# Performance work log

Hardware: AMD Instinct MI355X
Metric: run time of the kernel (lower is better)

Reference implementation:

```python
import jax, jax.numpy as jnp
import numpy as np

B, L = 16, 54            # dialogues, utterances per dialogue
NDIM = 512; H = 512; NS = 2
T = B * L                # 864 utterances
N = 3 * T                # 2592 nodes (l,a,v per utterance)
NE = B * (L + 3)         # 912 hyperedges (3 modality + L utterance per dialogue)
NNZ = 6 * T              # 5184 incidence entries
E = B * 3 * L * (L - 1)  # 137376 directed intra-modality edges
NUM_L = 3; NUM_K = 4
EPS = 1e-8


def _build_indices():
    rng = np.random.default_rng(0)
    spk = rng.integers(0, NS, size=(B, L))
    # qmask [L, B, NS] one-hot of speakers (matches torch argmax path)
    qmask = np.eye(NS, dtype=np.float32)[spk].transpose(1, 0, 2)
    ar = np.arange(L)
    i1, i2, ht = [], [], []
    for d in range(B):
        base = d * 3 * L
        nl = base + ar; na = nl + L; nv = nl + 2 * L
        # 3 modality hyperedges then L per-utterance (l,a,v) hyperedges
        i1 += [nl, na, nv, np.stack([nl, na, nv], 1).reshape(-1)]
        eb = d * (L + 3)
        i2 += [np.repeat(eb + np.arange(3), L), np.repeat(eb + 3 + ar, 3)]
        ht += [np.ones(L, np.int64), np.zeros(3, np.int64)]
    hyperedge_index = np.stack([np.concatenate(i1), np.concatenate(i2)]).astype(np.int64)
    hyperedge_type = np.concatenate(ht)
    # full permutation edges within each modality of each dialogue
    s0 = np.repeat(ar, L); d0 = np.tile(ar, L)
    m = s0 != d0; s0, d0 = s0[m], d0[m]
    src, dst, et = [], [], []
    for d in range(B):
        same = (spk[d][s0] == spk[d][d0]).astype(np.int64)
        for mm in range(3):
            off = d * 3 * L + mm * L
            src.append(s0 + off); dst.append(d0 + off); et.append(same)
    edge_index = np.stack([np.concatenate(src), np.concatenate(dst)]).astype(np.int64)
    edge_type = np.concatenate(et)
    return qmask, hyperedge_index, hyperedge_type, edge_index, edge_type


def setup_inputs() -> dict:
    key = jax.random.key(0)
    ks = jax.random.split(key, 16)
    qmask, hei, het, ei, et = _build_indices()
    n = lambda k, s: jax.random.normal(k, s, dtype=jnp.float32)
    inp = {
        'a': n(ks[0], (T, NDIM)), 'v': n(ks[1], (T, NDIM)), 'l': n(ks[2], (T, NDIM)),
        'qmask': jnp.asarray(qmask),
        'spk_emb': n(ks[3], (NS, NDIM)) * 0.05,
        'fc1_W': n(ks[4], (NDIM, H)) * 0.05, 'fc1_b': jnp.zeros((H,), jnp.float32),
        'he_weight': jnp.ones((NE,), jnp.float32),
        'ew_weight': jnp.ones((NNZ,), jnp.float32),
        'he_attr1': jax.random.uniform(ks[5], (H,), dtype=jnp.float32),
        'he_attr2': jax.random.uniform(ks[6], (H,), dtype=jnp.float32),
        'hc_W': n(ks[7], (NUM_L, H, H)) * 0.05, 'hc_b': jnp.zeros((NUM_L, H), jnp.float32),
        'm3_W0': n(ks[8], (NUM_K, H, H)) * 0.05,
        'm3_W1': n(ks[9], (NUM_K, H, H)) * 0.05,
        'm3_Wself': n(ks[10], (NUM_K, H, H)) * 0.05,
        'm3_b': jnp.zeros((NUM_K, H), jnp.float32),
        'hyperedge_index': jnp.asarray(hei), 'hyperedge_type': jnp.asarray(het),
        'edge_index': jnp.asarray(ei), 'edge_type': jnp.asarray(et),
    }
    return inp


def reference(a, v, l, qmask, spk_emb, fc1_W, fc1_b, he_weight, ew_weight,
              he_attr1, he_attr2, hc_W, hc_b, m3_W0, m3_W1, m3_Wself, m3_b,
              hyperedge_index, hyperedge_type, edge_index, edge_type):
    seg = jax.ops.segment_sum
    # speaker embedding added to text modality (equal dia_len -> simple transpose)
    qm = qmask.transpose(1, 0, 2).reshape(T, NS)
    l = l + spk_emb[jnp.argmax(qm, axis=-1)]
    # per-dialogue node order: [l_d ; a_d ; v_d]
    feats = jnp.concatenate([l.reshape(B, L, NDIM), a.reshape(B, L, NDIM),
                             v.reshape(B, L, NDIM)], axis=1).reshape(N, NDIM)
    x1 = feats @ fc1_W + fc1_b
    node_i, edge_i = hyperedge_index[0], hyperedge_index[1]
    tfl = hyperedge_type.astype(x1.dtype)[:, None]
    edge_attr = he_attr1[None, :] * tfl + he_attr2[None, :] * (1.0 - tfl)  # [NE,H]
    out = x1
    for ll in range(NUM_L):  # hypergraph conv: gather->edge agg->scatter->linear
        de = seg(ew_weight, edge_i, num_segments=NE)
        e = seg(ew_weight[:, None] * out[node_i], edge_i, num_segments=NE)
        e = e / (de + EPS)[:, None] + edge_attr
        c = he_weight[edge_i]
        dn = seg(c, node_i, num_segments=N)
        agg = seg(c[:, None] * e[edge_i], node_i, num_segments=N) / (dn + EPS)[:, None]
        out = jax.nn.relu(agg @ hc_W[ll] + hc_b[ll])
    src, dst = edge_index[0], edge_index[1]
    same_spk = (edge_type == 1)[:, None]
    deg = seg(jnp.ones_like(dst, dtype=x1.dtype), dst, num_segments=N)
    gnn_out = x1
    denoise = jnp.float32(0.0)
    for kk in range(NUM_K):  # 2-relation RGCN-style denoise layer
        h0 = gnn_out @ m3_W0[kk]
        h1 = gnn_out @ m3_W1[kk]
        msg = jnp.where(same_spk, h1[src], h0[src])
        agg = seg(msg, dst, num_segments=N) / (deg + EPS)[:, None]
        f = jax.nn.relu(agg + gnn_out @ m3_Wself[kk] + m3_b[kk])
        denoise = jnp.mean(f * f)
        gnn_out = gnn_out + f
    return out + gnn_out, denoise
```

## Files before the change

### kernel.cpp

```cpp
#include <hip/hip_runtime.h>

typedef unsigned short ushort_t;
typedef __attribute__((ext_vector_type(4))) float f32x4;
typedef __attribute__((ext_vector_type(8))) short s16x8;
typedef __attribute__((ext_vector_type(8))) unsigned short u16x8;

#define NNODE 2592
#define MATSZ (512*512)
#define INV53 (1.0f/(53.0f + 1e-8f))

__device__ __forceinline__ ushort_t f2b(float f){
  union {unsigned int i; float f;} x; x.f = f;
  unsigned int r = (x.i + 0x7fffu + ((x.i>>16)&1u))>>16;
  return (ushort_t)r;
}

__device__ __forceinline__ void gemm32(const ushort_t* As,
    const ushort_t* W, int col0, f32x4 acc[2][2])
{
  const int tid = threadIdx.x;
  const int wave = tid>>6, lane = tid&63;
  const int ml = lane&15, quad = lane>>4;
  #pragma unroll
  for (int mf=0;mf<2;mf++)
    #pragma unroll
    for (int nf=0;nf<2;nf++) acc[mf][nf] = (f32x4){0.f,0.f,0.f,0.f};

  const ushort_t* bw0 = W + (size_t)(col0 + wave*32 + ml)*512 + quad*8;
  const ushort_t* bw1 = bw0 + (size_t)16*512;
  const int rsw = ml&7;
  #pragma unroll
  for (int ks=0; ks<16; ks++){
    const int chunk = ks*4 + quad;
    const int abase = (chunk>>3)*64 + (((chunk&7) ^ rsw)<<3);
    s16x8 a0 = *(const s16x8*)&As[(size_t)ml*512 + abase];
    s16x8 a1 = *(const s16x8*)&As[(size_t)(16+ml)*512 + abase];
    s16x8 b0 = *(const s16x8*)(bw0 + ks*32);
    s16x8 b1 = *(const s16x8*)(bw1 + ks*32);
    acc[0][0] = __builtin_amdgcn_mfma_f32_16x16x32_bf16(a0,b0,acc[0][0],0,0,0);
    acc[0][1] = __builtin_amdgcn_mfma_f32_16x16x32_bf16(a0,b1,acc[0][1],0,0,0);
    acc[1][0] = __builtin_amdgcn_mfma_f32_16x16x32_bf16(a1,b0,acc[1][0],0,0,0);
    acc[1][1] = __builtin_amdgcn_mfma_f32_16x16x32_bf16(a1,b1,acc[1][1],0,0,0);
  }
}

__device__ __forceinline__ void stageA_flat(ushort_t* As, const float* src, int r0){
  const int tid = threadIdx.x;
  int row = tid>>3, seg = tid&7;
  const float* p = src + (size_t)(r0+row)*512 + seg*64;
  int rsw = row&7;
  ushort_t* dstA = &As[row*512 + seg*64];
  #pragma unroll
  for (int j=0;j<8;j++){
    f32x4 xa = *(const f32x4*)(p+j*8), xb = *(const f32x4*)(p+j*8+4);
    u16x8 v;
    #pragma unroll
    for (int jj=0;jj<4;jj++){ v[jj]=f2b(xa[jj]); v[4+jj]=f2b(xb[jj]); }
    *(u16x8*)&dstA[(j ^ rsw)<<3] = v;
  }
}

__device__ __forceinline__ void transpose_tile(float (*tile)[65],
    const float* src, const float* src2, ushort_t* dst, int bx, int by)
{
  const int tid = threadIdx.x;
  int r0 = bx*64, c0 = by*64;
  #pragma unroll
  for (int j=0;j<4;j++){
    int idx = j*256 + tid;
    int r = idx>>4, c4 = (idx&15)*4;
    size_t off = (size_t)(r0+r)*512 + c0 + c4;
    f32x4 v = *(const f32x4*)&src[off];
    if (src2){
      f32x4 v2 = *(const f32x4*)&src2[off];
      #pragma unroll
      for (int jj=0;jj<4;jj++) v[jj] -= INV53 * v2[jj];
    }
    #pragma unroll
    for (int jj=0;jj<4;jj++) tile[r][c4+jj] = v[jj];
  }
  __syncthreads();
  #pragma unroll
  for (int j=0;j<2;j++){
    int idx = j*256 + tid;
    int c = idx>>3, r8 = (idx&7)*8;
    u16x8 v;
    #pragma unroll
    for (int tt=0;tt<8;tt++) v[tt] = f2b(tile[r8+tt][c]);
    *(u16x8*)&dst[(size_t)(c0+c)*512 + r0 + r8] = v;
  }
}

__global__ __launch_bounds__(256) void prep0_kernel(
    const float* __restrict__ fc1,
    const float* __restrict__ A_in, const float* __restrict__ V_in,
    const float* __restrict__ L_in, const float* __restrict__ qmask,
    const float* __restrict__ spk,
    ushort_t* __restrict__ WT, float* __restrict__ FS,
    float* __restrict__ cnts, float* __restrict__ acc,
    unsigned int* __restrict__ counter)
{
  __shared__ float tile[64][65];
  __shared__ unsigned char spks[54];
  const int tid = threadIdx.x;
  if (blockIdx.x >= 64){
    int d = blockIdx.x - 64;
    if (tid < 54)
      spks[tid] = qmask[(tid*16+d)*2+1] > qmask[(tid*16+d)*2];
    __syncthreads();
    float cnt1 = 0.f;
    #pragma unroll
    for (int i=0;i<54;i++) cnt1 += (float)spks[i];
    float cnt0 = 54.f - cnt1;
    int col = tid*2;
    #pragma unroll
    for (int m=0;m<3;m++){
      float s0x=0.f,s0y=0.f,s1x=0.f,s1y=0.f;
      const float* base = (m==0)?L_in:(m==1)?A_in:V_in;
      for (int i=0;i<54;i++){
        float2 x = *(const float2*)&base[(size_t)(d*54+i)*512 + col];
        if (spks[i]){ s1x+=x.x; s1y+=x.y; } else { s0x+=x.x; s0y+=x.y; }
      }
      if (m==0){
        float2 e0 = *(const float2*)&spk[col];
        float2 e1 = *(const float2*)&spk[512+col];
        s0x += cnt0*e0.x; s0y += cnt0*e0.y;
        s1x += cnt1*e1.x; s1y += cnt1*e1.y;
      }
      float2 o0; o0.x=s0x; o0.y=s0y;
      float2 o1; o1.x=s1x; o1.y=s1y;
      *(float2*)&FS[(size_t)(d*6+m*2  )*512 + col] = o0;
      *(float2*)&FS[(size_t)(d*6+m*2+1)*512 + col] = o1;
    }
    if (tid==0){ cnts[d*2]=cnt0; cnts[d*2+1]=cnt1; }
    return;
  }
  if (blockIdx.x==0 && tid==0){ *acc = 0.f; *counter = 0u; }
  int t = blockIdx.x;
  transpose_tile(tile, fc1, nullptr, WT, t>>3, t&7);
}

__global__ __launch_bounds__(256) void fc1_kernel(
    const float* __restrict__ A_in, const float* __restrict__ V_in,
    const float* __restrict__ L_in, const float* __restrict__ qmask,
    const float* __restrict__ spk, const ushort_t* __restrict__ WTc,
    ushort_t* __restrict__ WT,
    const float* __restrict__ hc, const float* __restrict__ m0,
    const float* __restrict__ m1, const float* __restrict__ ms,
    const float* __restrict__ fc1_b, float* __restrict__ X1,
    const float* __restrict__ FS, const float* __restrict__ cnts,
    float* __restrict__ Gs)
{
  __shared__ __align__(16) union {
    ushort_t As[32*512];
    float tile[64][65];
  } sm;
  const int b = blockIdx.x, tid = threadIdx.x;
  const int wave = tid>>6, lane = tid&63;
  const int ml = lane&15, quad = lane>>4;
  if (b >= 336){
    const int bb = b - 336;
    const int w = 1 + (bb>>6), t = bb&63;
    const float* src = (w<4)  ? hc + (size_t)(w-1)*MATSZ
                     : (w<8)  ? m0 + (size_t)(w-4)*MATSZ
                     : (w<12) ? m1 + (size_t)(w-8)*MATSZ
                              : ms + (size_t)(w-12)*MATSZ;
    const float* src2 = (w>=12) ? m1 + (size_t)(w-12)*MATSZ : nullptr;
    transpose_tile(sm.tile, src, src2, WT + (size_t)w*MATSZ, t>>3, t&7);
    return;
  }
  if (b < 324){
    const int r0 = (b>>2)*32, col0 = (b&3)*128;
    {
      int row = tid>>3, seg = tid&7, gr = r0+row;
      int d = gr/162, rm = gr-d*162, m = rm/54, i = rm-m*54, t = d*54+i;
      const float* pa = ((m==0)?L_in:(m==1)?A_in:V_in) + (size_t)t*512 + seg*64;
      const float* pb = pa;
      bool hassp = (m==0);
      if (hassp){
        int sp = qmask[(i*16+d)*2+1] > qmask[(i*16+d)*2];
        pb = spk + sp*512 + seg*64;
      }
      int rsw = row&7;
      ushort_t* dstA = &sm.As[row*512 + seg*64];
      #pragma unroll
      for (int j=0;j<8;j++){
        f32x4 xa = *(const f32x4*)(pa+j*8), xb = *(const f32x4*)(pa+j*8+4);
        if (hassp){
          f32x4 ya = *(const f32x4*)(pb+j*8), yb = *(const f32x4*)(pb+j*8+4);
          #pragma unroll
          for (int jj=0;jj<4;jj++){ xa[jj]+=ya[jj]; xb[jj]+=yb[jj]; }
        }
        u16x8 v;
        #pragma unroll
        for (int jj=0;jj<4;jj++){ v[jj]=f2b(xa[jj]); v[4+jj]=f2b(xb[jj]); }
        *(u16x8*)&dstA[(j ^ rsw)<<3] = v;
      }
    }
    __syncthreads();
    f32x4 acc[2][2];
    gemm32(sm.As, WTc, col0, acc);
    #pragma unroll
    for (int nf=0;nf<2;nf++){
      int col = col0 + wave*32 + nf*16 + ml;
      float bv = fc1_b[col];
      #pragma unroll
      for (int mf=0;mf<2;mf++)
        #pragma unroll
        for (int r=0;r<4;r++){
          int gr = r0 + mf*16 + quad*4 + r;
          X1[(size_t)gr*512 + col] = acc[mf][nf][r] + bv;
        }
    }
  } else {
    const int bb = b-324;
    const int r0 = (bb>>2)*32, col0 = (bb&3)*128;
    stageA_flat(sm.As, FS, r0);
    __syncthreads();
    f32x4 acc[2][2];
    gemm32(sm.As, WTc, col0, acc);
    #pragma unroll
    for (int nf=0;nf<2;nf++){
      int col = col0 + wave*32 + nf*16 + ml;
      float bv = fc1_b[col];
      #pragma unroll
      for (int mf=0;mf<2;mf++)
        #pragma unroll
        for (int r=0;r<4;r++){
          int gr = r0 + mf*16 + quad*4 + r;
          float cw = cnts[(gr/6)*2 + (gr&1)];
          Gs[(size_t)gr*512 + col] = acc[mf][nf][r] + cw*bv;
        }
    }
  }
}

__global__ __launch_bounds__(256) void ka_kernel(int kk,
    const float* __restrict__ gin, const float* __restrict__ Gs,
    const ushort_t* __restrict__ WT, const float* __restrict__ m3_b,
    float* __restrict__ HS, float* __restrict__ Sp,
    const float* __restrict__ edge_src, const float* __restrict__ ew_w,
    const int* __restrict__ het, const float* __restrict__ attr1,
    const float* __restrict__ attr2, float* __restrict__ EB)
{
  __shared__ __align__(16) ushort_t As[32*512];
  const int b = blockIdx.x, tid = threadIdx.x;
  const int wave = tid>>6, lane = tid&63;
  const int ml = lane&15, quad = lane>>4;
  if (b < 324){
    const int r0 = (b>>2)*32, col0 = (b&3)*128;
    stageA_flat(As, gin, r0);
    __syncthreads();
    f32x4 acc[2][2];
    gemm32(As, WT + (size_t)(12+kk)*MATSZ, col0, acc);
    #pragma unroll
    for (int nf=0;nf<2;nf++){
      int col = col0 + wave*32 + nf*16 + ml;
      float bv = m3_b[kk*512 + col];
      #pragma unroll
      for (int mf=0;mf<2;mf++)
        #pragma unroll
        for (int r=0;r<4;r++){
          int gr = r0 + mf*16 + quad*4 + r;
          HS[(size_t)gr*512 + col] = acc[mf][nf][r] + bv;
        }
    }
  } else if (b < 348){
    const int bb = b-324;
    const int rt = bb>>3, c8 = bb&7;
    const int r0 = rt*32, col0 = (c8&3)*128;
    const ushort_t* W = WT + (size_t)((c8<4 ? 4 : 8)+kk)*MATSZ;
    const int cb = (c8<4) ? 0 : 512;
    stageA_flat(As, Gs, r0);
    __syncthreads();
    f32x4 acc[2][2];
    gemm32(As, W, col0, acc);
    #pragma unroll
    for (int nf=0;nf<2;nf++){
      int col = cb + col0 + wave*32 + nf*16 + ml;
      #pragma unroll
      for (int mf=0;mf<2;mf++)
        #pragma unroll
        for (int r=0;r<4;r++){
          int row = r0 + mf*16 + quad*4 + r;
          Sp[(size_t)row*1024 + col] = acc[mf][nf][r];
        }
    }
  } else {
    int e = b - 348;
    int d = e/57, r = e - d*57;
    int col = tid*2;
    float sx=0.f, sy=0.f, de=0.f;
    if (r < 3){
      int nnz0 = d*324 + r*54;
      const float* row = edge_src + ((size_t)(d*162 + r*54))*512 + col;
      for (int i=0;i<54;i++){
        float w = ew_w[nnz0+i];
        float2 x = *(const float2*)row;
        sx += w*x.x; sy += w*x.y; de += w;
        row += 512;
      }
    } else {
      int i = r-3;
      int nnz0 = d*324 + 162 + i*3;
      #pragma unroll
      for (int m=0;m<3;m++){
        float w = ew_w[nnz0+m];
        const float* row = edge_src + ((size_t)(d*162 + m*54 + i))*512 + col;
        float2 x = *(const float2*)row;
        sx += w*x.x; sy += w*x.y; de += w;
      }
    }
    float invde = 1.0f/(de + 1e-8f);
    const float* at = het[e] ? attr1 : attr2;
    float2 o;
    o.x = sx*invde + at[col];
    o.y = sy*invde + at[col+1];
    *(float2*)(EB + (size_t)e*512 + col) = o;
  }
}

template<bool LAST>
__global__ __launch_bounds__(256) void kb_kernel(int lk,
    const float* __restrict__ EB, const ushort_t* __restrict__ WT,
    const float* __restrict__ hc_b, float* __restrict__ dst,
    const float* __restrict__ gin, const float* __restrict__ HS,
    const float* __restrict__ Sp, const float* __restrict__ qmask,
    const float* __restrict__ he_w,
    float* __restrict__ Gout, float* __restrict__ GsOut,
    const float* __restrict__ OUThg, float* __restrict__ dout,
    float* __restrict__ accp, unsigned int* __restrict__ counter)
{
  __shared__ __align__(16) union {
    ushort_t As[32*512];
    struct { unsigned char spks[54]; float red[256]; } sf;
  } sm;
  const int b = blockIdx.x, tid = threadIdx.x;
  if (!LAST && b < 324){
    const int r0 = (b>>2)*32, col0 = (b&3)*128;
    {
      int row = tid>>3, seg = tid&7, gr = r0+row;
      int d = gr/162, rm = gr-d*162, m = rm/54, i = rm-m*54;
      int em = d*57+m, eu = d*57+3+i;
      float w1 = he_w[em], w2 = he_w[eu], inv = 1.0f/(w1+w2+1e-8f);
      float c1 = w1*inv, c2 = w2*inv;
      const float* pa = EB + (size_t)em*512 + seg*64;
      const float* pb = EB + (size_t)eu*512 + seg*64;
      int rsw = row&7;
      ushort_t* dstA = &sm.As[row*512 + seg*64];
      #pragma unroll
      for (int j=0;j<8;j++){
        f32x4 xa = *(const f32x4*)(pa+j*8), xb = *(const f32x4*)(pa+j*8+4);
        f32x4 ya = *(const f32x4*)(pb+j*8), yb = *(const f32x4*)(pb+j*8+4);
        u16x8 v;
        #pragma unroll
        for (int jj=0;jj<4;jj++){
          v[jj]   = f2b(c1*xa[jj] + c2*ya[jj]);
          v[4+jj] = f2b(c1*xb[jj] + c2*yb[jj]);
        }
        *(u16x8*)&dstA[(j ^ rsw)<<3] = v;
      }
    }
    __syncthreads();
    f32x4 acc[2][2];
    gemm32(sm.As, WT + (size_t)(1+lk)*MATSZ, col0, acc);
    const int wave = tid>>6, lane = tid&63;
    const int ml = lane&15, quad = lane>>4;
    #pragma unroll
    for (int nf=0;nf<2;nf++){
      int col = col0 + wave*32 + nf*16 + ml;
      float bv = hc_b[lk*512 + col];
      #pragma unroll
      for (int mf=0;mf<2;mf++)
        #pragma unroll
        for (int r=0;r<4;r++){
          int gr = r0 + mf*16 + quad*4 + r;
          dst[(size_t)gr*512 + col] = fmaxf(acc[mf][nf][r] + bv, 0.f);
        }
    }
  } else {
    const int sfid = LAST ? b : b-324;
    const int g = sfid>>1, d = g/3;
    const int col = (sfid&1)*256 + tid;
    if (tid < 54)
      sm.sf.spks[tid] = qmask[(tid*16+d)*2+1] > qmask[(tid*16+d)*2];
    __syncthreads();
    const float* r0p = Sp + (size_t)(g*2)*1024;
    const float* r1p = Sp + (size_t)(g*2+1)*1024;
    float S1_0 = r0p[512+col];
    float S1_1 = r1p[512+col];
    float S0_0 = r1p[col];
    float S0_1 = r0p[col];
    size_t base = (size_t)g*54*512 + col;
    float gs0=0.f, gs1=0.f, sumsq=0.f;
    for (int i=0;i<54;i++){
      size_t off = base + (size_t)i*512;
      int sp = sm.sf.spks[i];
      float S1 = sp ? S1_1 : S1_0;
      float S0 = sp ? S0_1 : S0_0;
      float hs = HS[off], gi = gin[off];
      float f = fmaxf((S1 + S0)*INV53 + hs, 0.f);
      float gn = gi + f;
      if (LAST){
        sumsq += f*f;
        dout[off] = OUThg[off] + gn;
      } else {
        Gout[off] = gn;
        if (sp) gs1 += gn; else gs0 += gn;
      }
    }
    if (!LAST){
      GsOut[(size_t)(g*2)*512 + col]   = gs0;
      GsOut[(size_t)(g*2+1)*512 + col] = gs1;
    } else {
      sm.sf.red[tid] = sumsq;
      __syncthreads();
      #pragma unroll
      for (int s=128; s>0; s>>=1){
        if (tid < s) sm.sf.red[tid] += sm.sf.red[tid+s];
        __syncthreads();
      }
      if (tid == 0){
        atomicAdd(accp, sm.sf.red[0]);
        __threadfence();
        unsigned int old = atomicAdd(counter, 1u);
        if (old == 95u)
          dout[(size_t)NNODE*512] = atomicAdd(accp, 0.0f) * (1.0f/1327104.0f);
      }
    }
  }
}

extern "C" void kernel_launch(void* const* d_in, const int* in_sizes, int n_in,
                              void* d_out, int out_size, void* d_ws, size_t ws_size,
                              hipStream_t stream)
{
  const float* A_in   = (const float*)d_in[0];
  const float* V_in   = (const float*)d_in[1];
  const float* L_in   = (const float*)d_in[2];
  const float* qmask  = (const float*)d_in[3];
  const float* spk    = (const float*)d_in[4];
  const float* fc1_W  = (const float*)d_in[5];
  const float* fc1_b  = (const float*)d_in[6];
  const float* he_w   = (const float*)d_in[7];
  const float* ew_w   = (const float*)d_in[8];
  const float* attr1  = (const float*)d_in[9];
  const float* attr2  = (const float*)d_in[10];
  const float* hc_W   = (const float*)d_in[11];
  const float* hc_b   = (const float*)d_in[12];
  const float* m3_W0  = (const float*)d_in[13];
  const float* m3_W1  = (const float*)d_in[14];
  const float* m3_Ws  = (const float*)d_in[15];
  const float* m3_b   = (const float*)d_in[16];
  const int*   het    = (const int*)d_in[18];
  float* dout = (float*)d_out;

  char* ws = (char*)d_ws;
  ushort_t* WT = (ushort_t*)ws;
  float* X1 = (float*)(ws + (size_t)16*MATSZ*2);
  float* OA = X1 + (size_t)NNODE*512;
  float* OB = OA + (size_t)NNODE*512;
  float* OC = OB + (size_t)NNODE*512;
  float* GA = OC + (size_t)NNODE*512;
  float* GB = GA + (size_t)NNODE*512;
  float* HS = GB + (size_t)NNODE*512;
  float* EB = HS + (size_t)NNODE*512;
  float* Sp = EB + (size_t)912*512;
  float* Gs = Sp + 96*1024;
  float* FS = Gs + 96*512;
  float* cnts = FS + 96*512;
  float* acc = cnts + 32;
  unsigned int* counter = (unsigned int*)(acc + 1);

  prep0_kernel<<<80,256,0,stream>>>(fc1_W, A_in, V_in, L_in, qmask, spk,
                                    WT, FS, cnts, acc, counter);
  fc1_kernel<<<1296,256,0,stream>>>(A_in, V_in, L_in, qmask, spk, WT, WT,
                                    hc_W, m3_W0, m3_W1, m3_Ws, fc1_b,
                                    X1, FS, cnts, Gs);

  ka_kernel<<<1260,256,0,stream>>>(0, X1, Gs, WT, m3_b, HS, Sp,
                                   X1, ew_w, het, attr1, attr2, EB);
  kb_kernel<false><<<420,256,0,stream>>>(0, EB, WT, hc_b, OA, X1, HS, Sp,
      qmask, he_w, GA, Gs, nullptr, nullptr, acc, counter);
  ka_kernel<<<1260,256,0,stream>>>(1, GA, Gs, WT, m3_b, HS, Sp,
                                   OA, ew_w, het, attr1, attr2, EB);
  kb_kernel<false><<<420,256,0,stream>>>(1, EB, WT, hc_b, OB, GA, HS, Sp,
      qmask, he_w, GB, Gs, nullptr, nullptr, acc, counter);
  ka_kernel<<<1260,256,0,stream>>>(2, GB, Gs, WT, m3_b, HS, Sp,
                                   OB, ew_w, het, attr1, attr2, EB);
  kb_kernel<false><<<420,256,0,stream>>>(2, EB, WT, hc_b, OC, GB, HS, Sp,
      qmask, he_w, GA, Gs, nullptr, nullptr, acc, counter);
  ka_kernel<<<348,256,0,stream>>>(3, GA, Gs, WT, m3_b, HS, Sp,
                                  X1, ew_w, het, attr1, attr2, EB);
  kb_kernel<true><<<96,256,0,stream>>>(3, EB, WT, hc_b, nullptr, GA, HS, Sp,
      qmask, he_w, nullptr, nullptr, OC, dout, acc, counter);

  (void)in_sizes; (void)n_in; (void)out_size; (void)ws_size;
}
```

Baseline: 296.3 us.

## Defer hypergraph-conv weight transposes into first ka launch and split prep0 per modality

The transposes of the three hc_W weight matrices move out of fc1_kernel and into extra blocks of the first ka_kernel launch, which does not use them. This shortens the fc1 launch and overlaps that conversion work with the ka GEMMs, since kb_kernel is the first consumer. The prep0 speaker-sum blocks are also split per (dialogue, modality) with two independent accumulator chains, raising parallelism from 16 to 48 blocks. The cost is a larger first ka grid, shared-memory union changes, and WT being written through a second alias in the same launch that reads other WT slices.

```diff
diff --git a/kernel.cpp b/kernel.cpp
--- a/kernel.cpp
+++ b/kernel.cpp
@@ -103,8 +103,9 @@
   __shared__ float tile[64][65];
   __shared__ unsigned char spks[54];
   const int tid = threadIdx.x;
-  if (blockIdx.x >= 64){
-    int d = blockIdx.x - 64;
+  if (blockIdx.x < 48){
+    if (blockIdx.x==0 && tid==0){ *acc = 0.f; *counter = 0u; }
+    const int d = blockIdx.x/3, m = blockIdx.x - d*3;
     if (tid < 54)
       spks[tid] = qmask[(tid*16+d)*2+1] > qmask[(tid*16+d)*2];
     __syncthreads();
@@ -112,31 +113,31 @@
     #pragma unroll
     for (int i=0;i<54;i++) cnt1 += (float)spks[i];
     float cnt0 = 54.f - cnt1;
-    int col = tid*2;
-    #pragma unroll
-    for (int m=0;m<3;m++){
-      float s0x=0.f,s0y=0.f,s1x=0.f,s1y=0.f;
-      const float* base = (m==0)?L_in:(m==1)?A_in:V_in;
-      for (int i=0;i<54;i++){
-        float2 x = *(const float2*)&base[(size_t)(d*54+i)*512 + col];
-        if (spks[i]){ s1x+=x.x; s1y+=x.y; } else { s0x+=x.x; s0y+=x.y; }
-      }
-      if (m==0){
-        float2 e0 = *(const float2*)&spk[col];
-        float2 e1 = *(const float2*)&spk[512+col];
-        s0x += cnt0*e0.x; s0y += cnt0*e0.y;
-        s1x += cnt1*e1.x; s1y += cnt1*e1.y;
-      }
-      float2 o0; o0.x=s0x; o0.y=s0y;
-      float2 o1; o1.x=s1x; o1.y=s1y;
-      *(float2*)&FS[(size_t)(d*6+m*2  )*512 + col] = o0;
-      *(float2*)&FS[(size_t)(d*6+m*2+1)*512 + col] = o1;
-    }
-    if (tid==0){ cnts[d*2]=cnt0; cnts[d*2+1]=cnt1; }
+    const int col = tid*2;
+    const float* base = (m==0)?L_in:(m==1)?A_in:V_in;
+    float a0x=0.f,a0y=0.f,a1x=0.f,a1y=0.f;
+    float b0x=0.f,b0y=0.f,b1x=0.f,b1y=0.f;
+    for (int i=0;i<27;i++){
+      float2 xa = *(const float2*)&base[(size_t)(d*54+i)*512 + col];
+      float2 xb = *(const float2*)&base[(size_t)(d*54+i+27)*512 + col];
+      if (spks[i])    { a1x+=xa.x; a1y+=xa.y; } else { a0x+=xa.x; a0y+=xa.y; }
+      if (spks[i+27]) { b1x+=xb.x; b1y+=xb.y; } else { b0x+=xb.x; b0y+=xb.y; }
+    }
+    float s0x=a0x+b0x, s0y=a0y+b0y, s1x=a1x+b1x, s1y=a1y+b1y;
+    if (m==0){
+      float2 e0 = *(const float2*)&spk[col];
+      float2 e1 = *(const float2*)&spk[512+col];
+      s0x += cnt0*e0.x; s0y += cnt0*e0.y;
+      s1x += cnt1*e1.x; s1y += cnt1*e1.y;
+    }
+    float2 o0; o0.x=s0x; o0.y=s0y;
+    float2 o1; o1.x=s1x; o1.y=s1y;
+    *(float2*)&FS[(size_t)(d*6+m*2  )*512 + col] = o0;
+    *(float2*)&FS[(size_t)(d*6+m*2+1)*512 + col] = o1;
+    if (m==0 && tid==0){ cnts[d*2]=cnt0; cnts[d*2+1]=cnt1; }
     return;
   }
-  if (blockIdx.x==0 && tid==0){ *acc = 0.f; *counter = 0u; }
-  int t = blockIdx.x;
+  const int t = blockIdx.x - 48;
   transpose_tile(tile, fc1, nullptr, WT, t>>3, t&7);
 }
 
@@ -145,8 +146,8 @@
     const float* __restrict__ L_in, const float* __restrict__ qmask,
     const float* __restrict__ spk, const ushort_t* __restrict__ WTc,
     ushort_t* __restrict__ WT,
-    const float* __restrict__ hc, const float* __restrict__ m0,
-    const float* __restrict__ m1, const float* __restrict__ ms,
+    const float* __restrict__ m0, const float* __restrict__ m1,
+    const float* __restrict__ ms,
     const float* __restrict__ fc1_b, float* __restrict__ X1,
     const float* __restrict__ FS, const float* __restrict__ cnts,
     float* __restrict__ Gs)
@@ -160,9 +161,8 @@
   const int ml = lane&15, quad = lane>>4;
   if (b >= 336){
     const int bb = b - 336;
-    const int w = 1 + (bb>>6), t = bb&63;
-    const float* src = (w<4)  ? hc + (size_t)(w-1)*MATSZ
-                     : (w<8)  ? m0 + (size_t)(w-4)*MATSZ
+    const int w = 4 + (bb>>6), t = bb&63;
+    const float* src = (w<8)  ? m0 + (size_t)(w-4)*MATSZ
                      : (w<12) ? m1 + (size_t)(w-8)*MATSZ
                               : ms + (size_t)(w-12)*MATSZ;
     const float* src2 = (w>=12) ? m1 + (size_t)(w-12)*MATSZ : nullptr;
@@ -241,18 +241,29 @@
     float* __restrict__ HS, float* __restrict__ Sp,
     const float* __restrict__ edge_src, const float* __restrict__ ew_w,
     const int* __restrict__ het, const float* __restrict__ attr1,
-    const float* __restrict__ attr2, float* __restrict__ EB)
-{
-  __shared__ __align__(16) ushort_t As[32*512];
+    const float* __restrict__ attr2, float* __restrict__ EB,
+    const float* __restrict__ hcW, ushort_t* __restrict__ WTmut)
+{
+  __shared__ __align__(16) union {
+    ushort_t As[32*512];
+    float tile[64][65];
+  } sm;
   const int b = blockIdx.x, tid = threadIdx.x;
   const int wave = tid>>6, lane = tid&63;
   const int ml = lane&15, quad = lane>>4;
+  if (b >= 1260){
+    const int bb = b - 1260;
+    const int w = 1 + (bb>>6), t = bb&63;
+    transpose_tile(sm.tile, hcW + (size_t)(w-1)*MATSZ, nullptr,
+                   WTmut + (size_t)w*MATSZ, t>>3, t&7);
+    return;
+  }
   if (b < 324){
     const int r0 = (b>>2)*32, col0 = (b&3)*128;
-    stageA_flat(As, gin, r0);
+    stageA_flat(sm.As, gin, r0);
     __syncthreads();
     f32x4 acc[2][2];
-    gemm32(As, WT + (size_t)(12+kk)*MATSZ, col0, acc);
+    gemm32(sm.As, WT + (size_t)(12+kk)*MATSZ, col0, acc);
     #pragma unroll
     for (int nf=0;nf<2;nf++){
       int col = col0 + wave*32 + nf*16 + ml;
@@ -271,10 +282,10 @@
     const int r0 = rt*32, col0 = (c8&3)*128;
     const ushort_t* W = WT + (size_t)((c8<4 ? 4 : 8)+kk)*MATSZ;
     const int cb = (c8<4) ? 0 : 512;
-    stageA_flat(As, Gs, r0);
+    stageA_flat(sm.As, Gs, r0);
     __syncthreads();
     f32x4 acc[2][2];
-    gemm32(As, W, col0, acc);
+    gemm32(sm.As, W, col0, acc);
     #pragma unroll
     for (int nf=0;nf<2;nf++){
       int col = cb + col0 + wave*32 + nf*16 + ml;
@@ -472,26 +483,26 @@
   float* acc = cnts + 32;
   unsigned int* counter = (unsigned int*)(acc + 1);
 
-  prep0_kernel<<<80,256,0,stream>>>(fc1_W, A_in, V_in, L_in, qmask, spk,
-                                    WT, FS, cnts, acc, counter);
-  fc1_kernel<<<1296,256,0,stream>>>(A_in, V_in, L_in, qmask, spk, WT, WT,
-                                    hc_W, m3_W0, m3_W1, m3_Ws, fc1_b,
+  prep0_kernel<<<112,256,0,stream>>>(fc1_W, A_in, V_in, L_in, qmask, spk,
+                                     WT, FS, cnts, acc, counter);
+  fc1_kernel<<<1104,256,0,stream>>>(A_in, V_in, L_in, qmask, spk, WT, WT,
+                                    m3_W0, m3_W1, m3_Ws, fc1_b,
                                     X1, FS, cnts, Gs);
 
-  ka_kernel<<<1260,256,0,stream>>>(0, X1, Gs, WT, m3_b, HS, Sp,
-                                   X1, ew_w, het, attr1, attr2, EB);
+  ka_kernel<<<1452,256,0,stream>>>(0, X1, Gs, WT, m3_b, HS, Sp,
+                                   X1, ew_w, het, attr1, attr2, EB, hc_W, WT);
   kb_kernel<false><<<420,256,0,stream>>>(0, EB, WT, hc_b, OA, X1, HS, Sp,
       qmask, he_w, GA, Gs, nullptr, nullptr, acc, counter);
   ka_kernel<<<1260,256,0,stream>>>(1, GA, Gs, WT, m3_b, HS, Sp,
-                                   OA, ew_w, het, attr1, attr2, EB);
+                                   OA, ew_w, het, attr1, attr2, EB, hc_W, WT);
   kb_kernel<false><<<420,256,0,stream>>>(1, EB, WT, hc_b, OB, GA, HS, Sp,
       qmask, he_w, GB, Gs, nullptr, nullptr, acc, counter);
   ka_kernel<<<1260,256,0,stream>>>(2, GB, Gs, WT, m3_b, HS, Sp,
-                                   OB, ew_w, het, attr1, attr2, EB);
+                                   OB, ew_w, het, attr1, attr2, EB, hc_W, WT);
   kb_kernel<false><<<420,256,0,stream>>>(2, EB, WT, hc_b, OC, GB, HS, Sp,
       qmask, he_w, GA, Gs, nullptr, nullptr, acc, counter);
   ka_kernel<<<348,256,0,stream>>>(3, GA, Gs, WT, m3_b, HS, Sp,
-                                  X1, ew_w, het, attr1, attr2, EB);
+                                  X1, ew_w, het, attr1, attr2, EB, hc_W, WT);
   kb_kernel<true><<<96,256,0,stream>>>(3, EB, WT, hc_b, nullptr, GA, HS, Sp,
       qmask, he_w, nullptr, nullptr, OC, dout, acc, counter);
 
```

Result: faster. 252.3 us (-14.8%).
